# Performance work log

Measured on AMD Instinct MI355X. Metric: run time of the kernel, lower is better.

The kernel has to match this reference:

```python
import jax, jax.numpy as jnp
import numpy as np

N_EMBD = 1024
HEADS = 16
HEAD_DIM = N_EMBD // HEADS


def setup_inputs() -> dict:
    key = jax.random.key(0)
    k1, k2 = jax.random.split(key)
    x = jax.random.normal(k1, (2, 2048, N_EMBD), dtype=jnp.float32)
    W_qkv = jax.random.normal(k2, (N_EMBD, 3 * N_EMBD), dtype=jnp.float32) * (N_EMBD ** -0.5)
    b_qkv = jnp.zeros((3 * N_EMBD,), dtype=jnp.float32)
    return {"x": x, "W_qkv": W_qkv, "b_qkv": b_qkv}


def reference(x, W_qkv, b_qkv):
    B, T, _ = x.shape
    qkv = x @ W_qkv + b_qkv                      # [B, T, 3*n_embd]
    q, k, v = jnp.split(qkv, 3, axis=-1)
    q = q.reshape(B, T, HEADS, HEAD_DIM)
    k = k.reshape(B, T, HEADS, HEAD_DIM)
    v = v.reshape(B, T, HEADS, HEAD_DIM)
    attn = jnp.einsum('bthd,bThd->bhtT', q, k) / jnp.sqrt(jnp.float32(HEAD_DIM))
    causal = jnp.tril(jnp.ones((T, T), dtype=bool))  # [T, T]
    attn = jnp.where(causal, attn, -jnp.inf)
    attn = jax.nn.softmax(attn, axis=-1)
    # dropout is identity in deterministic/eval mode (training=False)
    out = jnp.einsum('bhtT,bThd->bthd', attn, v).reshape(B, T, N_EMBD)
    return out
```

## Files before the change

### kernel.cpp

```cpp
#include <hip/hip_runtime.h>
#include <hip/hip_bf16.h>

#define BATCH 2
#define TSEQ  2048
#define NEMBD 1024
#define HEADS 16
#define HDIM  64

typedef short          bf16x8 __attribute__((ext_vector_type(8)));
typedef float          f32x4  __attribute__((ext_vector_type(4)));
typedef unsigned short u16;

__device__ __forceinline__ u16 f2bf(float f) {
  unsigned int u = __float_as_uint(f);
  u += 0x7fffu + ((u >> 16) & 1u);
  return (u16)(u >> 16);
}

__device__ __forceinline__ unsigned int cvt_pk_bf16(float lo, float hi) {
  unsigned int r;
  asm("v_cvt_pk_bf16_f32 %0, %1, %2" : "=v"(r) : "v"(lo), "v"(hi));
  return r;
}

__device__ __forceinline__ void gld16(const u16* g, u16* l) {
  __builtin_amdgcn_global_load_lds(
      (const __attribute__((address_space(1))) unsigned int*)g,
      (__attribute__((address_space(3))) unsigned int*)l, 16, 0, 0);
}

__global__ __launch_bounds__(256) void k_prep(const float* __restrict__ x,
                                              u16* __restrict__ xb,
                                              const float* __restrict__ w,
                                              u16* __restrict__ wt) {
  __shared__ float tile[32][33];
  const int b = blockIdx.x;
  const int t = threadIdx.x;
  if (b < 4096) {
    int i = b * 256 + t;
    float4 v = ((const float4*)x)[i];
    ushort4 o;
    o.x = f2bf(v.x); o.y = f2bf(v.y); o.z = f2bf(v.z); o.w = f2bf(v.w);
    ((ushort4*)xb)[i] = o;
  } else {
    const int bt = b - 4096;
    const int n0 = (bt >> 5) * 32;
    const int k0 = (bt & 31) * 32;
    const int r  = t >> 3;
    const int c4 = (t & 7) * 4;
    float4 v = *(const float4*)(w + (size_t)(k0 + r) * 3072 + n0 + c4);
    tile[r][c4 + 0] = v.x; tile[r][c4 + 1] = v.y;
    tile[r][c4 + 2] = v.z; tile[r][c4 + 3] = v.w;
    __syncthreads();
    ushort4 o;
    o.x = f2bf(tile[c4 + 0][r]);
    o.y = f2bf(tile[c4 + 1][r]);
    o.z = f2bf(tile[c4 + 2][r]);
    o.w = f2bf(tile[c4 + 3][r]);
    *(ushort4*)(wt + (size_t)(n0 + r) * 1024 + k0 + c4) = o;
  }
}

__global__ __launch_bounds__(256, 3) void k_qkv_gemm(
    const u16* __restrict__ xb, const u16* __restrict__ wt,
    const float* __restrict__ bias,
    u16* __restrict__ qb, u16* __restrict__ kbuf, u16* __restrict__ vt) {
  __shared__ __align__(16) u16 As[128 * 64];
  __shared__ __align__(16) u16 Bs[128 * 64];

  const int t    = threadIdx.x;
  const int wv   = t >> 6;
  const int lane = t & 63;
  const int m    = lane & 15;
  const int quad = lane >> 4;
  const int lin  = blockIdx.x;
  const int cp   = lin >> 5;
  const int rp   = ((lin & 7) << 2) | ((lin >> 3) & 3);
  const int row0 = rp * 128;
  const int col0 = cp * 128;
  const int wr   = (wv >> 1) * 64;
  const int wc   = (wv & 1) * 64;

  const int sr = wv * 32 + (lane >> 3);
  const int gs = (lane & 7) ^ (sr & 7);
  const u16* ag = xb + (size_t)(row0 + sr) * 1024 + gs * 8;
  const u16* bg = wt + (size_t)(col0 + sr) * 1024 + gs * 8;
  u16* al = As + (wv * 32) * 64;
  u16* bl = Bs + (wv * 32) * 64;

  f32x4 acc[4][4];
  const f32x4 zf = {0.f, 0.f, 0.f, 0.f};
  for (int i = 0; i < 4; ++i)
    for (int j = 0; j < 4; ++j) acc[i][j] = zf;

  for (int kt = 0; kt < 16; ++kt) {
    const int kk = kt * 64;
    __syncthreads();
    gld16(ag + kk,             al);
    gld16(ag + kk +  8 * 1024, al +  8 * 64);
    gld16(ag + kk + 16 * 1024, al + 16 * 64);
    gld16(ag + kk + 24 * 1024, al + 24 * 64);
    gld16(bg + kk,             bl);
    gld16(bg + kk +  8 * 1024, bl +  8 * 64);
    gld16(bg + kk + 16 * 1024, bl + 16 * 64);
    gld16(bg + kk + 24 * 1024, bl + 24 * 64);
    __syncthreads();

#pragma unroll
    for (int h = 0; h < 2; ++h) {
      const int g = ((quad + 4 * h) ^ (m & 7)) * 8;
      bf16x8 af[4], bfr[4];
#pragma unroll
      for (int mt = 0; mt < 4; ++mt)
        af[mt] = *(const bf16x8*)(As + (wr + mt * 16 + m) * 64 + g);
#pragma unroll
      for (int nt = 0; nt < 4; ++nt)
        bfr[nt] = *(const bf16x8*)(Bs + (wc + nt * 16 + m) * 64 + g);
#pragma unroll
      for (int mt = 0; mt < 4; ++mt)
#pragma unroll
        for (int nt = 0; nt < 4; ++nt)
          acc[mt][nt] = __builtin_amdgcn_mfma_f32_16x16x32_bf16(
              af[mt], bfr[nt], acc[mt][nt], 0, 0, 0);
    }
  }

  const int sec = col0 >> 10;
#pragma unroll
  for (int nt = 0; nt < 4; ++nt) {
    const int Cc = col0 + wc + nt * 16 + m;
    const float bv = bias[Cc];
    const int c = Cc & 1023;
    const int h = c >> 6;
    const int d = c & 63;
#pragma unroll
    for (int mt = 0; mt < 4; ++mt) {
      const int Rbase = row0 + wr + mt * 16 + quad * 4;
      const int bb = Rbase >> 11;
      const int t0 = Rbase & 2047;
      const int bh = bb * HEADS + h;
      if (sec == 0) {
#pragma unroll
        for (int rg = 0; rg < 4; ++rg) {
          float v = (acc[mt][nt][rg] + bv) * 0.125f;
          qb[(size_t)(bh * TSEQ + t0 + rg) * HDIM + d] = f2bf(v);
        }
      } else if (sec == 1) {
#pragma unroll
        for (int rg = 0; rg < 4; ++rg) {
          float v = acc[mt][nt][rg] + bv;
          kbuf[(size_t)(bh * TSEQ + t0 + rg) * HDIM + d] = f2bf(v);
        }
      } else {
        uint2 pk;
        pk.x = cvt_pk_bf16(acc[mt][nt][0] + bv, acc[mt][nt][1] + bv);
        pk.y = cvt_pk_bf16(acc[mt][nt][2] + bv, acc[mt][nt][3] + bv);
        *(uint2*)(vt + (size_t)(bh * HDIM + d) * TSEQ + t0) = pk;
      }
    }
  }
}

__global__ __launch_bounds__(256, 3) void k_attn(
    const u16* __restrict__ qb, const u16* __restrict__ kbuf,
    const u16* __restrict__ vt, float* __restrict__ out) {
  __shared__ __align__(16) u16 Kb[2][4096];
  __shared__ __align__(16) u16 Vb[2][4096];
  __shared__ __align__(16) u16 pt[4][16 * 72];

  const int t     = threadIdx.x;
  const int wv    = t >> 6;
  const int lane  = t & 63;
  const int m     = lane & 15;
  const int quad  = lane >> 4;
  const int bh    = blockIdx.x & 31;
  const int qtg   = 31 - (blockIdx.x >> 5);
  const int qbase = (qtg * 4 + wv) * 16;
  const int nkt   = qtg + 1;

  u16* pw = &pt[wv][0];

  const u16* qrow = qb + ((size_t)bh * TSEQ + qbase + m) * HDIM + quad * 8;
  bf16x8 aq0 = *(const bf16x8*)(qrow);
  bf16x8 aq1 = *(const bf16x8*)(qrow + 32);

  const int sr = wv * 16 + (lane >> 3);
  const int gsk = (lane & 7) ^ (sr & 7);
  const u16* kg = kbuf + ((size_t)bh * TSEQ + sr) * HDIM + gsk * 8;
  const u16* vg = vt + ((size_t)bh * HDIM + sr) * TSEQ + gsk * 8;
  u16* klds = &Kb[0][wv * 16 * 64];
  u16* vlds = &Vb[0][wv * 16 * 64];

  const int swL = (quad ^ (m & 7)) * 8;
  const int swH = ((quad + 4) ^ (m & 7)) * 8;

  f32x4 o[4];
  const f32x4 zf = {0.f, 0.f, 0.f, 0.f};
  for (int nt = 0; nt < 4; ++nt) o[nt] = zf;
  float rsum = 0.f;
  const int qi = qbase + m;

  gld16(kg,             klds);
  gld16(kg + 8 * HDIM,  klds + 8 * 64);
  gld16(vg,             vlds);
  gld16(vg + 8 * TSEQ,  vlds + 8 * 64);
  __syncthreads();

  for (int kt = 0; kt < nkt; ++kt) {
    const int b = kt & 1;
    const u16* kb0 = &Kb[b][0];
    const u16* vb0 = &Vb[b][0];

    f32x4 s[4];
    for (int nt = 0; nt < 4; ++nt) s[nt] = zf;
#pragma unroll
    for (int nt = 0; nt < 4; ++nt) {
      bf16x8 kf = *(const bf16x8*)(kb0 + (nt * 16 + m) * 64 + swL);
      s[nt] = __builtin_amdgcn_mfma_f32_16x16x32_bf16(kf, aq0, s[nt], 0, 0, 0);
    }
#pragma unroll
    for (int nt = 0; nt < 4; ++nt) {
      bf16x8 kf = *(const bf16x8*)(kb0 + (nt * 16 + m) * 64 + swH);
      s[nt] = __builtin_amdgcn_mfma_f32_16x16x32_bf16(kf, aq1, s[nt], 0, 0, 0);
    }

    bf16x8 vfL[4], vfH[4];
#pragma unroll
    for (int nt = 0; nt < 4; ++nt) {
      vfL[nt] = *(const bf16x8*)(vb0 + (nt * 16 + m) * 64 + swL);
      vfH[nt] = *(const bf16x8*)(vb0 + (nt * 16 + m) * 64 + swH);
    }

    if (kt + 1 < nkt) {
      const int nb = (kt + 1) & 1;
      const u16* kgn = kg + (size_t)(kt + 1) * 64 * HDIM;
      const u16* vgn = vg + (kt + 1) * 64;
      u16* kl = &Kb[nb][wv * 16 * 64];
      u16* vl = &Vb[nb][wv * 16 * 64];
      gld16(kgn,            kl);
      gld16(kgn + 8 * HDIM, kl + 8 * 64);
      gld16(vgn,            vl);
      gld16(vgn + 8 * TSEQ, vl + 8 * 64);
    }

    if (kt == nkt - 1) {
      const int kb = kt * 64 + quad * 4;
#pragma unroll
      for (int nt = 0; nt < 4; ++nt)
#pragma unroll
        for (int rg = 0; rg < 4; ++rg)
          if (kb + nt * 16 + rg > qi) s[nt][rg] = -1e30f;
    }

#pragma unroll
    for (int nt = 0; nt < 4; ++nt) {
      float p0 = __expf(s[nt][0]), p1 = __expf(s[nt][1]);
      float p2 = __expf(s[nt][2]), p3 = __expf(s[nt][3]);
      rsum += (p0 + p1) + (p2 + p3);
      uint2 pk;
      pk.x = cvt_pk_bf16(p0, p1);
      pk.y = cvt_pk_bf16(p2, p3);
      *(uint2*)(pw + m * 72 + nt * 16 + quad * 4) = pk;
    }
    bf16x8 bp0 = *(const bf16x8*)(pw + m * 72 + quad * 8);
    bf16x8 bp1 = *(const bf16x8*)(pw + m * 72 + 32 + quad * 8);

#pragma unroll
    for (int nt = 0; nt < 4; ++nt)
      o[nt] = __builtin_amdgcn_mfma_f32_16x16x32_bf16(vfL[nt], bp0, o[nt], 0, 0, 0);
#pragma unroll
    for (int nt = 0; nt < 4; ++nt)
      o[nt] = __builtin_amdgcn_mfma_f32_16x16x32_bf16(vfH[nt], bp1, o[nt], 0, 0, 0);

    __syncthreads();
  }

  rsum += __shfl_xor(rsum, 16);
  rsum += __shfl_xor(rsum, 32);
  const float inv = 1.0f / rsum;

  const int bb = bh >> 4;
  const int h  = bh & 15;
  float* ob = out + ((size_t)(bb * TSEQ + qi) * NEMBD + h * HDIM + quad * 4);
#pragma unroll
  for (int nt = 0; nt < 4; ++nt) {
    float4 st;
    st.x = o[nt][0] * inv; st.y = o[nt][1] * inv;
    st.z = o[nt][2] * inv; st.w = o[nt][3] * inv;
    *(float4*)(ob + nt * 16) = st;
  }
}

extern "C" void kernel_launch(void* const* d_in, const int* in_sizes, int n_in,
                              void* d_out, int out_size, void* d_ws, size_t ws_size,
                              hipStream_t stream) {
  (void)in_sizes; (void)n_in; (void)out_size; (void)ws_size;
  const float* x    = (const float*)d_in[0];
  const float* W    = (const float*)d_in[1];
  const float* bqkv = (const float*)d_in[2];
  float* out = (float*)d_out;

  u16* ws   = (u16*)d_ws;
  u16* qb   = ws;
  u16* kbuf = ws + 4194304;
  u16* vt   = ws + 2 * 4194304;
  u16* xb   = ws + 3 * 4194304;
  u16* wt   = ws + 4 * 4194304;

  hipLaunchKernelGGL(k_prep, dim3(7168), dim3(256), 0, stream, x, xb, W, wt);
  hipLaunchKernelGGL(k_qkv_gemm, dim3(768), dim3(256), 0, stream,
                     xb, wt, bqkv, qb, kbuf, vt);
  hipLaunchKernelGGL(k_attn, dim3(1024), dim3(256), 0, stream,
                     qb, kbuf, vt, out);
}
```

Before: 140.2 us.

## Unroll attention loop by two with static LDS buffers, early prefetch, exp2 softmax

Splits the double-buffered K/V LDS arrays into separate static buffers and unrolls the key-tile loop by two through a macro, so buffer addresses become compile-time constants. The prefetch of the next tile is issued at the start of each tile instead of after the score MFMAs, giving the loads more time to overlap compute. The log2(e) factor is folded into the Q scale so the softmax can use exp2f. The risk is higher register pressure and code size from the duplicated tile body.

```diff
diff --git a/kernel.cpp b/kernel.cpp
--- a/kernel.cpp
+++ b/kernel.cpp
@@ -142,7 +142,7 @@
       if (sec == 0) {
 #pragma unroll
         for (int rg = 0; rg < 4; ++rg) {
-          float v = (acc[mt][nt][rg] + bv) * 0.125f;
+          float v = (acc[mt][nt][rg] + bv) * 0.18033688f;
           qb[(size_t)(bh * TSEQ + t0 + rg) * HDIM + d] = f2bf(v);
         }
       } else if (sec == 1) {
@@ -164,8 +164,10 @@
 __global__ __launch_bounds__(256, 3) void k_attn(
     const u16* __restrict__ qb, const u16* __restrict__ kbuf,
     const u16* __restrict__ vt, float* __restrict__ out) {
-  __shared__ __align__(16) u16 Kb[2][4096];
-  __shared__ __align__(16) u16 Vb[2][4096];
+  __shared__ __align__(16) u16 Kb0[4096];
+  __shared__ __align__(16) u16 Kb1[4096];
+  __shared__ __align__(16) u16 Vb0[4096];
+  __shared__ __align__(16) u16 Vb1[4096];
   __shared__ __align__(16) u16 pt[4][16 * 72];
 
   const int t     = threadIdx.x;
@@ -188,8 +190,6 @@
   const int gsk = (lane & 7) ^ (sr & 7);
   const u16* kg = kbuf + ((size_t)bh * TSEQ + sr) * HDIM + gsk * 8;
   const u16* vg = vt + ((size_t)bh * HDIM + sr) * TSEQ + gsk * 8;
-  u16* klds = &Kb[0][wv * 16 * 64];
-  u16* vlds = &Vb[0][wv * 16 * 64];
 
   const int swL = (quad ^ (m & 7)) * 8;
   const int swH = ((quad + 4) ^ (m & 7)) * 8;
@@ -200,80 +200,84 @@
   float rsum = 0.f;
   const int qi = qbase + m;
 
-  gld16(kg,             klds);
-  gld16(kg + 8 * HDIM,  klds + 8 * 64);
-  gld16(vg,             vlds);
-  gld16(vg + 8 * TSEQ,  vlds + 8 * 64);
+#define ATTN_TILE(KB, VB, DODMA, TN, NKL, NVL, DOMASK)                        \
+  {                                                                           \
+    if (DODMA) {                                                              \
+      const u16* kgn = kg + (size_t)(TN) * 64 * HDIM;                         \
+      const u16* vgn = vg + (TN) * 64;                                        \
+      gld16(kgn,            (NKL));                                           \
+      gld16(kgn + 8 * HDIM, (NKL) + 8 * 64);                                  \
+      gld16(vgn,            (NVL));                                           \
+      gld16(vgn + 8 * TSEQ, (NVL) + 8 * 64);                                  \
+    }                                                                         \
+    f32x4 s[4];                                                               \
+    for (int nt = 0; nt < 4; ++nt) s[nt] = zf;                                \
+    _Pragma("unroll")                                                         \
+    for (int nt = 0; nt < 4; ++nt) {                                          \
+      bf16x8 kf = *(const bf16x8*)((KB) + (nt * 16 + m) * 64 + swL);          \
+      s[nt] = __builtin_amdgcn_mfma_f32_16x16x32_bf16(kf, aq0, s[nt], 0,0,0); \
+    }                                                                         \
+    _Pragma("unroll")                                                         \
+    for (int nt = 0; nt < 4; ++nt) {                                          \
+      bf16x8 kf = *(const bf16x8*)((KB) + (nt * 16 + m) * 64 + swH);          \
+      s[nt] = __builtin_amdgcn_mfma_f32_16x16x32_bf16(kf, aq1, s[nt], 0,0,0); \
+    }                                                                         \
+    bf16x8 vfL[4], vfH[4];                                                    \
+    _Pragma("unroll")                                                         \
+    for (int nt = 0; nt < 4; ++nt) {                                          \
+      vfL[nt] = *(const bf16x8*)((VB) + (nt * 16 + m) * 64 + swL);            \
+      vfH[nt] = *(const bf16x8*)((VB) + (nt * 16 + m) * 64 + swH);            \
+    }                                                                         \
+    if (DOMASK) {                                                             \
+      const int kb_ = (nkt - 1) * 64 + quad * 4;                              \
+      _Pragma("unroll")                                                       \
+      for (int nt = 0; nt < 4; ++nt)                                          \
+        _Pragma("unroll")                                                     \
+        for (int rg = 0; rg < 4; ++rg)                                        \
+          if (kb_ + nt * 16 + rg > qi) s[nt][rg] = -1e30f;                    \
+    }                                                                         \
+    _Pragma("unroll")                                                         \
+    for (int nt = 0; nt < 4; ++nt) {                                          \
+      float p0 = exp2f(s[nt][0]), p1 = exp2f(s[nt][1]);                       \
+      float p2 = exp2f(s[nt][2]), p3 = exp2f(s[nt][3]);                       \
+      rsum += (p0 + p1) + (p2 + p3);                                          \
+      uint2 pk;                                                               \
+      pk.x = cvt_pk_bf16(p0, p1);                                             \
+      pk.y = cvt_pk_bf16(p2, p3);                                             \
+      *(uint2*)(pw + m * 72 + nt * 16 + quad * 4) = pk;                       \
+    }                                                                         \
+    bf16x8 bp0 = *(const bf16x8*)(pw + m * 72 + quad * 8);                    \
+    bf16x8 bp1 = *(const bf16x8*)(pw + m * 72 + 32 + quad * 8);               \
+    _Pragma("unroll")                                                         \
+    for (int nt = 0; nt < 4; ++nt)                                            \
+      o[nt] = __builtin_amdgcn_mfma_f32_16x16x32_bf16(vfL[nt], bp0, o[nt],    \
+                                                      0, 0, 0);               \
+    _Pragma("unroll")                                                         \
+    for (int nt = 0; nt < 4; ++nt)                                            \
+      o[nt] = __builtin_amdgcn_mfma_f32_16x16x32_bf16(vfH[nt], bp1, o[nt],    \
+                                                      0, 0, 0);               \
+  }
+
+  gld16(kg,            &Kb0[wv * 16 * 64]);
+  gld16(kg + 8 * HDIM, &Kb0[wv * 16 * 64 + 8 * 64]);
+  gld16(vg,            &Vb0[wv * 16 * 64]);
+  gld16(vg + 8 * TSEQ, &Vb0[wv * 16 * 64 + 8 * 64]);
   __syncthreads();
 
-  for (int kt = 0; kt < nkt; ++kt) {
-    const int b = kt & 1;
-    const u16* kb0 = &Kb[b][0];
-    const u16* vb0 = &Vb[b][0];
-
-    f32x4 s[4];
-    for (int nt = 0; nt < 4; ++nt) s[nt] = zf;
-#pragma unroll
-    for (int nt = 0; nt < 4; ++nt) {
-      bf16x8 kf = *(const bf16x8*)(kb0 + (nt * 16 + m) * 64 + swL);
-      s[nt] = __builtin_amdgcn_mfma_f32_16x16x32_bf16(kf, aq0, s[nt], 0, 0, 0);
-    }
-#pragma unroll
-    for (int nt = 0; nt < 4; ++nt) {
-      bf16x8 kf = *(const bf16x8*)(kb0 + (nt * 16 + m) * 64 + swH);
-      s[nt] = __builtin_amdgcn_mfma_f32_16x16x32_bf16(kf, aq1, s[nt], 0, 0, 0);
-    }
-
-    bf16x8 vfL[4], vfH[4];
-#pragma unroll
-    for (int nt = 0; nt < 4; ++nt) {
-      vfL[nt] = *(const bf16x8*)(vb0 + (nt * 16 + m) * 64 + swL);
-      vfH[nt] = *(const bf16x8*)(vb0 + (nt * 16 + m) * 64 + swH);
-    }
-
-    if (kt + 1 < nkt) {
-      const int nb = (kt + 1) & 1;
-      const u16* kgn = kg + (size_t)(kt + 1) * 64 * HDIM;
-      const u16* vgn = vg + (kt + 1) * 64;
-      u16* kl = &Kb[nb][wv * 16 * 64];
-      u16* vl = &Vb[nb][wv * 16 * 64];
-      gld16(kgn,            kl);
-      gld16(kgn + 8 * HDIM, kl + 8 * 64);
-      gld16(vgn,            vl);
-      gld16(vgn + 8 * TSEQ, vl + 8 * 64);
-    }
-
-    if (kt == nkt - 1) {
-      const int kb = kt * 64 + quad * 4;
-#pragma unroll
-      for (int nt = 0; nt < 4; ++nt)
-#pragma unroll
-        for (int rg = 0; rg < 4; ++rg)
-          if (kb + nt * 16 + rg > qi) s[nt][rg] = -1e30f;
-    }
-
-#pragma unroll
-    for (int nt = 0; nt < 4; ++nt) {
-      float p0 = __expf(s[nt][0]), p1 = __expf(s[nt][1]);
-      float p2 = __expf(s[nt][2]), p3 = __expf(s[nt][3]);
-      rsum += (p0 + p1) + (p2 + p3);
-      uint2 pk;
-      pk.x = cvt_pk_bf16(p0, p1);
-      pk.y = cvt_pk_bf16(p2, p3);
-      *(uint2*)(pw + m * 72 + nt * 16 + quad * 4) = pk;
-    }
-    bf16x8 bp0 = *(const bf16x8*)(pw + m * 72 + quad * 8);
-    bf16x8 bp1 = *(const bf16x8*)(pw + m * 72 + 32 + quad * 8);
-
-#pragma unroll
-    for (int nt = 0; nt < 4; ++nt)
-      o[nt] = __builtin_amdgcn_mfma_f32_16x16x32_bf16(vfL[nt], bp0, o[nt], 0, 0, 0);
-#pragma unroll
-    for (int nt = 0; nt < 4; ++nt)
-      o[nt] = __builtin_amdgcn_mfma_f32_16x16x32_bf16(vfH[nt], bp1, o[nt], 0, 0, 0);
-
-    __syncthreads();
-  }
+  int kt = 0;
+  for (; kt + 1 < nkt; kt += 2) {
+    ATTN_TILE(&Kb0[0], &Vb0[0], true, kt + 1,
+              &Kb1[wv * 16 * 64], &Vb1[wv * 16 * 64], false)
+    __syncthreads();
+    ATTN_TILE(&Kb1[0], &Vb1[0], (kt + 2 < nkt), kt + 2,
+              &Kb0[wv * 16 * 64], &Vb0[wv * 16 * 64], (kt + 2 >= nkt))
+    __syncthreads();
+  }
+  if (kt < nkt) {
+    ATTN_TILE(&Kb0[0], &Vb0[0], false, 0,
+              &Kb1[wv * 16 * 64], &Vb1[wv * 16 * 64], true)
+  }
+#undef ATTN_TILE
 
   rsum += __shfl_xor(rsum, 16);
   rsum += __shfl_xor(rsum, 32);
```

Result: no change. 140.8 us (+0.5%).
